# Optimization experiments

Hardware: AMD Instinct MI355X
Metric: run time of the kernel (lower is better)

Reference implementation:

```python
import jax, jax.numpy as jnp
import numpy as np

B, L, DIN, D = 16, 4096, 64, 64
HA, HL, WIN, NL, K, DFF = 8, 4, 64, 3, 3, 128


def _ln(x, g, b):
    m = x.mean(-1, keepdims=True)
    v = ((x - m) ** 2).mean(-1, keepdims=True)
    return (x - m) * jax.lax.rsqrt(v + 1e-5) * g + b


def _dynamic_conv(x, kernels, w1, b1, w2, b2):
    # x: (B, C, H, 1); kernels: (K, C_out, C_in, 3, 3)
    b, c, h, w = x.shape
    pooled = x.mean(axis=(2, 3))                      # AdaptiveAvgPool2d(1)
    hdn = jax.nn.relu(pooled @ w1.T + b1)             # 1x1 conv C -> C//4
    attn = jax.nn.softmax(hdn @ w2.T + b2, axis=-1)   # (B, K) kernel weights
    kw = kernels.reshape(K * c, c, 3, 3)              # run all K kernels in one conv
    out = jax.lax.conv_general_dilated(x, kw, (1, 1), [(1, 1), (1, 1)],
                                       dimension_numbers=('NCHW', 'OIHW', 'NCHW'))
    out = out.reshape(b, K, c, h, w)
    return jnp.einsum('bkchw,bk->bchw', out, attn)


def _agent_attn(x, wv, bv, an_bias, na_bias):
    # agent_num = 1: a single pooled agent token per sample
    b, n, c = x.shape
    hd = c // HA
    scale = hd ** -0.5
    v = x @ wv + bv
    lepe = v                                          # get_lepe uses the same linear
    qh = x.reshape(b, n, HA, hd).transpose(0, 2, 1, 3)  # (B, HA, L, hd)
    kh = qh
    vh = v.reshape(b, n, HA, hd).transpose(0, 2, 1, 3)
    agent = x.mean(axis=1).reshape(b, HA, 1, hd)      # AdaptiveAvgPool1d(1) over L
    a_attn = jax.nn.softmax(jnp.einsum('bhad,bhnd->bhan', agent * scale, kh) + an_bias, axis=-1)
    agent_v = jnp.einsum('bhan,bhnd->bhad', a_attn, vh)            # (B, HA, 1, hd)
    nb = jnp.swapaxes(na_bias, -1, -2)                              # (HA, L, 1)
    q_attn = jax.nn.softmax(jnp.einsum('bhnd,bhad->bhna', qh * scale, agent) + nb, axis=-1)
    out = jnp.einsum('bhna,bhad->bhnd', q_attn, agent_v)
    return out.transpose(0, 2, 1, 3).reshape(b, n, c) + lepe


def _local_attn(x, wq, bq, wk, bk, wv, bv, wo, bo):
    b, n, d = x.shape
    dk = d // HL
    nw = n // WIN

    def heads(w, bias):
        return (x @ w + bias).reshape(b, nw, WIN, HL, dk).transpose(0, 3, 1, 2, 4)

    q, k, v = heads(wq, bq), heads(wk, bk), heads(wv, bv)
    s = jnp.einsum('bhwid,bhwjd->bhwij', q, k) / (dk ** 0.5)        # per-window scores
    a = jax.nn.softmax(s, axis=-1)
    o = jnp.einsum('bhwij,bhwjd->bhwid', a, v)
    o = o.transpose(0, 2, 3, 1, 4).reshape(b, n, d)
    return o @ wo + bo


def setup_inputs() -> dict:
    key = jax.random.key(0)
    ks = iter(jax.random.split(key, 40))
    nrm = lambda shape, s=0.02: jax.random.normal(next(ks), shape, jnp.float32) * s
    Cr = DIN // 4
    return {
        'x': jax.random.normal(next(ks), (B, L, DIN), jnp.float32),
        'dc_kernels': nrm((3, K, DIN, DIN, 3, 3), 0.05),
        'dc_w1': nrm((3, Cr, DIN)), 'dc_b1': jnp.zeros((3, Cr), jnp.float32),
        'dc_w2': nrm((3, K, Cr)), 'dc_b2': jnp.zeros((3, K), jnp.float32),
        'emb_w': nrm((DIN, D)), 'emb_b': jnp.zeros((D,), jnp.float32),
        'getv_w': nrm((NL, D, D)), 'getv_b': jnp.zeros((NL, D), jnp.float32),
        'an_bias': nrm((NL, HA, 1, L)), 'na_bias': nrm((NL, HA, 1, L)),
        'wq': nrm((NL, D, D)), 'bq': jnp.zeros((NL, D), jnp.float32),
        'wk': nrm((NL, D, D)), 'bk': jnp.zeros((NL, D), jnp.float32),
        'wv': nrm((NL, D, D)), 'bv': jnp.zeros((NL, D), jnp.float32),
        'wo': nrm((NL, D, D)), 'bo': jnp.zeros((NL, D), jnp.float32),
        'ff_w1': nrm((NL, D, DFF)), 'ff_b1': jnp.zeros((NL, DFF), jnp.float32),
        'ff_w2': nrm((NL, DFF, D)), 'ff_b2': jnp.zeros((NL, D), jnp.float32),
        'ln1_g': jnp.ones((NL, D), jnp.float32), 'ln1_b': jnp.zeros((NL, D), jnp.float32),
        'ln2_g': jnp.ones((NL, D), jnp.float32), 'ln2_b': jnp.zeros((NL, D), jnp.float32),
    }


def reference(x, dc_kernels, dc_w1, dc_b1, dc_w2, dc_b2, emb_w, emb_b,
              getv_w, getv_b, an_bias, na_bias,
              wq, bq, wk, bk, wv, bv, wo, bo,
              ff_w1, ff_b1, ff_w2, ff_b2, ln1_g, ln1_b, ln2_g, ln2_b):
    # dynamic multi-kernel convs on (B, C=d_input, H=L, W=1)
    h = x.transpose(0, 2, 1)[..., None]
    for i in range(3):
        h = _dynamic_conv(h, dc_kernels[i], dc_w1[i], dc_b1[i], dc_w2[i], dc_b2[i])
    h = h[..., 0].transpose(0, 2, 1)
    # data embedding (value_linear=True, value_sqrt=False, pos_emb=False)
    h = h @ emb_w + emb_b
    for i in range(NL):
        attn = _agent_attn(h, getv_w[i], getv_b[i], an_bias[i], na_bias[i]) + \
               _local_attn(h, wq[i], bq[i], wk[i], bk[i], wv[i], bv[i], wo[i], bo[i])
        h1 = _ln(h + attn, ln1_g[i], ln1_b[i])
        ffo = jax.nn.relu(h1 @ ff_w1[i] + ff_b1[i]) @ ff_w2[i] + ff_b2[i]
        h = _ln(h1 + ffo, ln2_g[i], ln2_b[i])
    return h
```

## Files before the change

kernel.cpp:

```cpp
#include <hip/hip_runtime.h>

#define BB 16
#define LL 4096
#define DD 64

typedef const float* __restrict__ cfp;
typedef float* __restrict__ fp;
typedef const ushort* __restrict__ cup;
typedef ushort* __restrict__ up;

typedef __attribute__((ext_vector_type(8))) short bf16x8;
typedef __attribute__((ext_vector_type(4))) float f32x4;
#define MFMA16(a, b, c) __builtin_amdgcn_mfma_f32_16x16x32_bf16(a, b, c, 0, 0, 0)

__device__ __forceinline__ f32x4 zf4(){ f32x4 z; z[0]=0.f; z[1]=0.f; z[2]=0.f; z[3]=0.f; return z; }

union frag_u { bf16x8 v; uint2 u2[2]; uint u[4]; };

__device__ __forceinline__ float4 ld4(const float* p){ return *reinterpret_cast<const float4*>(p); }

__device__ __forceinline__ ushort f2bf(float f){
  uint u = __float_as_uint(f);
  return (ushort)((u + 0x7FFFu + ((u >> 16) & 1u)) >> 16);
}
__device__ __forceinline__ float bf2f(ushort u){
  return __uint_as_float(((uint)u) << 16);
}
__device__ __forceinline__ uint packf2(float a, float b){
  return (uint)f2bf(a) | ((uint)f2bf(b) << 16);
}
__device__ __forceinline__ uint2 pack4(float4 v){
  return make_uint2(packf2(v.x, v.y), packf2(v.z, v.w));
}
__device__ __forceinline__ bf16x8 ldfrag(const ushort* p){ return *reinterpret_cast<const bf16x8*>(p); }

__global__ __launch_bounds__(256) void k_pack(cfp wq, cfp wk, cfp wv, cfp getv, cfp wo,
                                              cfp fw1, cfp fw2, cfp embw,
                                              up dst, up dstE) {
  int layer = blockIdx.y;
  int e = blockIdx.x*256 + threadIdx.x;
  if (e >= 36864) {
    int rem = e - 36864;
    int j = rem & 7, lane = (rem >> 3) & 63, rest = rem >> 9;
    int nt = rest & 3, ks = rest >> 2;
    int k = ks*32 + ((lane >> 4) << 3) + j, n = nt*16 + (lane & 15);
    dstE[rem] = f2bf(embw[k*64 + n]);
    return;
  }
  const float* W; int N, rem;
  if (e < 20480) {
    int mm = e >> 12; rem = e & 4095;
    W = (mm==0?wq: mm==1?wk: mm==2?wv: mm==3?getv: wo) + layer*4096; N = 64;
  } else if (e < 28672) {
    rem = e - 20480; W = fw1 + layer*8192; N = 128;
  } else {
    rem = e - 28672; W = fw2 + layer*8192; N = 64;
  }
  int NT = N >> 4;
  int j = rem & 7, lane = (rem >> 3) & 63, rest = rem >> 9;
  int nt = rest % NT, ks = rest / NT;
  int k = ks*32 + ((lane >> 4) << 3) + j, n = nt*16 + (lane & 15);
  dst[(size_t)layer*36864 + e] = f2bf(W[(size_t)k*N + n]);
}

__global__ __launch_bounds__(256) void k_pool_part(cfp h, fp pp) {
  int b = blockIdx.x, gblk = blockIdx.y, t = threadIdx.x;
  int c = t & 63, r = t >> 6;
  const float* base = h + ((size_t)b*LL + (size_t)gblk*256)*64;
  float acc = 0.f;
  for (int l = r; l < 256; l += 4) acc += base[(size_t)l*64 + c];
  __shared__ float red[4][64];
  red[r][c] = acc; __syncthreads();
  if (t < 64) pp[(b*16 + gblk)*64 + t] = red[0][t]+red[1][t]+red[2][t]+red[3][t];
}

__device__ __forceinline__ void tiny_mlp3(int t, const float* __restrict__ pooled,
                                          cfp w1, cfp b1, cfp w2, cfp b2,
                                          float* attn, float* hdn) {
  if (t < 16) {
    float a = b1[t];
    for (int c = 0; c < 64; ++c) a += pooled[c]*w1[t*64 + c];
    hdn[t] = fmaxf(a, 0.f);
  }
  __syncthreads();
  if (t < 3) {
    float a = b2[t];
    for (int j = 0; j < 16; ++j) a += hdn[j]*w2[t*16 + j];
    attn[t] = a;
  }
  __syncthreads();
  if (t == 0) {
    float m = fmaxf(attn[0], fmaxf(attn[1], attn[2]));
    float e0 = __expf(attn[0]-m), e1 = __expf(attn[1]-m), e2 = __expf(attn[2]-m);
    float s = e0+e1+e2;
    attn[0]=e0/s; attn[1]=e1/s; attn[2]=e2/s;
  }
  __syncthreads();
}

__global__ __launch_bounds__(256) void k_attns(cfp pp, cfp x, cfp dcw1, cfp dcb1,
                                               cfp dcw2, cfp dcb2, cfp dck, fp attns) {
  int b = blockIdx.x, t = threadIdx.x;
  __shared__ float S[64], e0v[64], e1v[64], em0[64], em1[64];
  __shared__ float h10[64], h1m[64], Sn[64];
  __shared__ float pooled[64], hdn[16], attn[3], redu[256];
  const float* xb = x + (size_t)b*LL*64;
  if (t < 64) {
    float s = 0.f;
    for (int g = 0; g < 16; ++g) s += pp[((size_t)b*16 + g)*64 + t];
    S[t] = s;
    pooled[t] = s * (1.f/4096.f);
    e0v[t] = xb[t];
    e1v[t] = xb[64 + t];
    em0[t] = xb[(size_t)(LL-2)*64 + t];
    em1[t] = xb[(size_t)(LL-1)*64 + t];
  }
  __syncthreads();
  tiny_mlp3(t, pooled, dcw1, dcb1, dcw2, dcb2, attn, hdn);
  if (t < 3) attns[b*9 + t] = attn[t];
  {
    int co = t & 63, q = t >> 6;
    float a0 = attn[0], a1 = attn[1], a2 = attn[2];
    float ph0=0.f, phm=0.f, pS=0.f;
    cfp kb = dck;
    for (int ci = q*16; ci < q*16 + 16; ++ci) {
      size_t base = ((size_t)co*64 + ci)*9 + 1;
      float k00=kb[base],       k01=kb[base+3],       k02=kb[base+6];
      float k10=kb[base+36864], k11=kb[base+36867],   k12=kb[base+36870];
      float k20=kb[base+73728], k21=kb[base+73731],   k22=kb[base+73734];
      float w0 = a0*k00 + a1*k10 + a2*k20;
      float w1 = a0*k01 + a1*k11 + a2*k21;
      float w2 = a0*k02 + a1*k12 + a2*k22;
      ph0 += w1*e0v[ci] + w2*e1v[ci];
      phm += w0*em0[ci] + w1*em1[ci];
      pS  += w0*(S[ci]-em1[ci]) + w1*S[ci] + w2*(S[ci]-e0v[ci]);
    }
    redu[t] = ph0; __syncthreads();
    if (t < 64) h10[t] = redu[t]+redu[64+t]+redu[128+t]+redu[192+t];
    __syncthreads();
    redu[t] = phm; __syncthreads();
    if (t < 64) h1m[t] = redu[t]+redu[64+t]+redu[128+t]+redu[192+t];
    __syncthreads();
    redu[t] = pS; __syncthreads();
    if (t < 64) {
      Sn[t] = redu[t]+redu[64+t]+redu[128+t]+redu[192+t];
      pooled[t] = Sn[t] * (1.f/4096.f);
    }
    __syncthreads();
  }
  tiny_mlp3(t, pooled, dcw1+1024, dcb1+16, dcw2+48, dcb2+3, attn, hdn);
  if (t < 3) attns[b*9 + 3 + t] = attn[t];
  {
    int co = t & 63, q = t >> 6;
    float a0 = attn[0], a1 = attn[1], a2 = attn[2];
    float pS = 0.f;
    cfp kb = dck + 110592;
    for (int ci = q*16; ci < q*16 + 16; ++ci) {
      size_t base = ((size_t)co*64 + ci)*9 + 1;
      float k00=kb[base],       k01=kb[base+3],       k02=kb[base+6];
      float k10=kb[base+36864], k11=kb[base+36867],   k12=kb[base+36870];
      float k20=kb[base+73728], k21=kb[base+73731],   k22=kb[base+73734];
      float w0 = a0*k00 + a1*k10 + a2*k20;
      float w1 = a0*k01 + a1*k11 + a2*k21;
      float w2 = a0*k02 + a1*k12 + a2*k22;
      pS += w0*(Sn[ci]-h1m[ci]) + w1*Sn[ci] + w2*(Sn[ci]-h10[ci]);
    }
    redu[t] = pS; __syncthreads();
    if (t < 64) pooled[t] = (redu[t]+redu[64+t]+redu[128+t]+redu[192+t]) * (1.f/4096.f);
    __syncthreads();
  }
  tiny_mlp3(t, pooled, dcw1+2048, dcb1+32, dcw2+96, dcb2+6, attn, hdn);
  if (t < 3) attns[b*9 + 6 + t] = attn[t];
}

__global__ __launch_bounds__(256) void k_wefff(cfp attns, cfp dck, up weffB) {
  int b = blockIdx.x, stage = blockIdx.y >> 3, slice = blockIdx.y & 7, t = threadIdx.x;
  float a0 = attns[b*9 + stage*3 + 0];
  float a1 = attns[b*9 + stage*3 + 1];
  float a2 = attns[b*9 + stage*3 + 2];
  cfp kern = dck + (size_t)stage*110592;
  int e0i = slice*1536;
  for (int e = e0i + t; e < e0i + 1536; e += 256) {
    int j = e & 7, lane = (e >> 3) & 63, nt = (e >> 9) & 3, ks = e >> 11;
    int k = ks*32 + ((lane >> 4) << 3) + j;
    int co = nt*16 + (lane & 15);
    int kh = k >> 6, ci = k & 63;
    size_t base = ((size_t)co*64 + ci)*9 + kh*3 + 1;
    float v = a0*kern[base] + a1*kern[base + 36864] + a2*kern[base + 2*36864];
    weffB[((size_t)stage*16 + b)*12288 + e] = f2bf(v);
  }
}

__device__ __forceinline__ void conv_mfma(const ushort* Ts, const ushort* wb,
                                          int band, int lr, int lg, int l, f32x4 acc[4]) {
  #pragma unroll
  for (int nt = 0; nt < 4; ++nt) acc[nt] = zf4();
  #pragma unroll
  for (int ks = 0; ks < 6; ++ks) {
    int k8 = ks*32 + lg*8;
    int kh = k8 >> 6, ci = k8 & 63;
    bf16x8 a = ldfrag(Ts + (band + lr + kh)*72 + ci);
    #pragma unroll
    for (int nt = 0; nt < 4; ++nt)
      acc[nt] = MFMA16(a, ldfrag(wb + ((ks*4+nt)*64 + l)*8), acc[nt]);
  }
}

__global__ __launch_bounds__(256) void k_convF(cfp x, cup weffB, cup wE, cfp embb,
                                               up houtB, fp pp) {
  int b = blockIdx.x, wblk = blockIdx.y, t = threadIdx.x;
  int n0 = wblk*64;
  __shared__ ushort TsA[84*72];
  __shared__ ushort TsB[84*72];
  __shared__ float red[64*17];
  int w = t >> 6, l = t & 63, lr = l & 15, lg = l >> 4;

  for (int idx = t; idx < 1344; idx += 256) {
    int r = idx >> 4, c4 = (idx & 15)*4;
    int g = n0 - 4 + r;
    float4 v = make_float4(0.f,0.f,0.f,0.f);
    if (r >= 1 && r <= 70 && g >= 0 && g < LL) v = ld4(x + ((size_t)b*LL + g)*64 + c4);
    *(uint2*)(TsA + r*72 + c4) = pack4(v);
  }
  for (int idx = t; idx < 32; idx += 256) {
    int r = 82 + (idx >> 4), c4 = (idx & 15)*4;
    *(uint2*)(TsB + r*72 + c4) = make_uint2(0u,0u);
  }
  __syncthreads();

  {
    const ushort* wb = weffB + (size_t)b*12288;
    for (int bi = w; bi < 5; bi += 4) {
      int band = 2 + bi*16;
      f32x4 acc[4];
      conv_mfma(TsA, wb, band - 1, lr, lg, l, acc);
      #pragma unroll
      for (int nt = 0; nt < 4; ++nt)
        #pragma unroll
        for (int reg = 0; reg < 4; ++reg) {
          int row = band + lg*4 + reg;
          int g = n0 - 4 + row;
          float v = (g >= 0 && g < LL) ? acc[nt][reg] : 0.f;
          TsB[row*72 + nt*16 + lr] = f2bf(v);
        }
    }
  }
  __syncthreads();
  {
    const ushort* wb = weffB + (size_t)(16 + b)*12288;
    for (int bi = w; bi < 5; bi += 4) {
      int band = 3 + bi*16;
      f32x4 acc[4];
      conv_mfma(TsB, wb, band - 1, lr, lg, l, acc);
      #pragma unroll
      for (int nt = 0; nt < 4; ++nt)
        #pragma unroll
        for (int reg = 0; reg < 4; ++reg) {
          int row = band + lg*4 + reg;
          int g = n0 - 4 + row;
          float v = (g >= 0 && g < LL) ? acc[nt][reg] : 0.f;
          TsA[row*72 + nt*16 + lr] = f2bf(v);
        }
    }
  }
  __syncthreads();
  {
    const ushort* wb = weffB + (size_t)(32 + b)*12288;
    int band = 4 + w*16;
    f32x4 acc[4];
    conv_mfma(TsA, wb, band - 1, lr, lg, l, acc);
    #pragma unroll
    for (int nt = 0; nt < 4; ++nt)
      #pragma unroll
      for (int reg = 0; reg < 4; ++reg)
        TsB[(band + lg*4 + reg)*72 + nt*16 + lr] = f2bf(acc[nt][reg]);
  }
  __syncthreads();
  {
    int band = 4 + w*16;
    f32x4 ea[4];
    #pragma unroll
    for (int nt = 0; nt < 4; ++nt) ea[nt] = zf4();
    #pragma unroll
    for (int ks = 0; ks < 2; ++ks) {
      bf16x8 a = ldfrag(TsB + (band + lr)*72 + ks*32 + lg*8);
      #pragma unroll
      for (int nt = 0; nt < 4; ++nt)
        ea[nt] = MFMA16(a, ldfrag(wE + ((ks*4+nt)*64 + l)*8), ea[nt]);
    }
    #pragma unroll
    for (int nt = 0; nt < 4; ++nt) {
      int col = nt*16 + lr;
      float bc = embb[col], part = 0.f;
      #pragma unroll
      for (int reg = 0; reg < 4; ++reg) {
        int row = band + lg*4 + reg;
        float y = ea[nt][reg] + bc;
        TsA[row*72 + col] = f2bf(y);
        part += y;
      }
      red[col*17 + w*4 + lg] = part;
    }
  }
  __syncthreads();
  for (int idx = t; idx < 512; idx += 256) {
    int r = idx >> 3, c8 = (idx & 7)*8;
    *(uint4*)(houtB + ((size_t)b*LL + n0 + r)*64 + c8) = *(const uint4*)(TsA + (r+4)*72 + c8);
  }
  if (t < 64) {
    float s = 0.f;
    #pragma unroll
    for (int g = 0; g < 16; ++g) s += red[t*17 + g];
    pp[((size_t)b*64 + wblk)*64 + t] = s;
  }
}

__global__ __launch_bounds__(256) void k_agent2(cup h16, cfp anb, cfp pp,
                                                fp pm, fp pe, fp pw) {
  int b = blockIdx.x, ch = blockIdx.y, t = threadIdx.x;
  int w = t >> 6, l = t & 63;
  __shared__ float means_s[64];
  __shared__ float sc[8][258];
  __shared__ float red4[4][64];
  __shared__ float esp[8][33];
  __shared__ float mcs[8], ess[8];
  __shared__ float wred[4][8][64];
  {
    float acc = 0.f;
    for (int c = w; c < 64; c += 4) acc += pp[((size_t)b*64 + c)*64 + l];
    red4[w][l] = acc;
  }
  __syncthreads();
  if (t < 64) means_s[t] = (red4[0][t]+red4[1][t]+red4[2][t]+red4[3][t])
                           * (1.f/4096.f) * 0.35355339059327373f;
  __syncthreads();
  const ushort* hb = h16 + ((size_t)b*LL + (size_t)ch*256)*64;
  int g8 = l >> 3, k8 = l & 7;
  float ms8[8];
  #pragma unroll
  for (int j = 0; j < 8; ++j) ms8[j] = means_s[k8*8 + j];
  #pragma unroll
  for (int it = 0; it < 8; ++it) {
    int n = w*64 + it*8 + g8;
    uint4 hv = *(const uint4*)(hb + (size_t)n*64 + k8*8);
    float d = bf2f((ushort)(hv.x & 0xffffu))*ms8[0] + bf2f((ushort)(hv.x >> 16))*ms8[1]
            + bf2f((ushort)(hv.y & 0xffffu))*ms8[2] + bf2f((ushort)(hv.y >> 16))*ms8[3]
            + bf2f((ushort)(hv.z & 0xffffu))*ms8[4] + bf2f((ushort)(hv.z >> 16))*ms8[5]
            + bf2f((ushort)(hv.w & 0xffffu))*ms8[6] + bf2f((ushort)(hv.w >> 16))*ms8[7];
    sc[k8][n] = d;
  }
  __syncthreads();
  int hh = t >> 5, j0 = (t & 31) * 8;
  const float* ab = anb + (size_t)hh*LL + ch*256 + j0;
  float loc[8];
  float mx = -1e30f;
  #pragma unroll
  for (int k = 0; k < 8; ++k) {
    loc[k] = sc[hh][j0 + k] + ab[k];
    mx = fmaxf(mx, loc[k]);
  }
  esp[hh][t & 31] = mx;
  __syncthreads();
  if (t < 8) {
    float m = -1e30f;
    for (int k = 0; k < 32; ++k) m = fmaxf(m, esp[t][k]);
    mcs[t] = m;
  }
  __syncthreads();
  {
    float M = mcs[hh], s = 0.f;
    #pragma unroll
    for (int k = 0; k < 8; ++k) {
      float e = __expf(loc[k] - M);
      sc[hh][j0 + k] = e;
      s += e;
    }
    esp[hh][t & 31] = s;
  }
  __syncthreads();
  if (t < 8) {
    float s = 0.f;
    for (int k = 0; k < 32; ++k) s += esp[t][k];
    ess[t] = s;
  }
  float acc8[8] = {};
  for (int i = 0; i < 64; ++i) {
    int n = w*64 + i;
    float xv = bf2f(hb[(size_t)n*64 + l]);
    #pragma unroll
    for (int q = 0; q < 8; ++q) acc8[q] = fmaf(sc[q][n], xv, acc8[q]);
  }
  __syncthreads();
  #pragma unroll
  for (int q = 0; q < 8; ++q) wred[w][q][l] = acc8[q];
  __syncthreads();
  for (int o = t; o < 512; o += 256) {
    int q = o >> 6, ll = o & 63;
    pw[(((size_t)b*16 + ch)*8 + q)*64 + ll] =
        wred[0][q][ll]+wred[1][q][ll]+wred[2][q][ll]+wred[3][q][ll];
  }
  if (t < 8) {
    pe[((size_t)b*16 + ch)*8 + t] = ess[t];
    pm[((size_t)b*16 + ch)*8 + t] = mcs[t];
  }
}

template<bool OUT_BF16>
__global__ __launch_bounds__(256, 4) void k_layer(
    cup h16, cfp pm, cfp pe, cfp pw, cfp getv, cfp getvb, cup wB,
    cfp bq, cfp bk, cfp bv, cfp bo,
    cfp g1, cfp be1, cfp b1, cfp b2, cfp g2, cfp be2,
    fp Y, up Y16, fp pp) {
  __shared__ float smem[10048];
  ushort* HsB  = (ushort*)(smem);
  ushort* Qp   = (ushort*)(smem + 2304);
  ushort* Kp   = (ushort*)(smem + 4864);
  ushort* Vt   = (ushort*)(smem + 7424);
  float*  sums = smem + 9728;
  float*  agvs = smem + 9984;
  float*  wm   = smem + 7424;
  float*  msden= smem + 7944;
  ushort* OB   = (ushort*)(smem + 7424);
  float*  red  = smem + 7424;
  ushort* HidB = (ushort*)(smem + 2304);

  int t = threadIdx.x;
  size_t n0 = (size_t)blockIdx.x*64;
  int b = (int)(n0 >> 12);
  int w = t >> 6, l = t & 63, band = w*16, lr = l & 15, lg = l >> 4;

  #pragma unroll
  for (int it = 0; it < 2; ++it) {
    int idx = it*256 + t, r = idx >> 3, c8 = (idx & 7)*8;
    *(uint4*)(HsB + r*72 + c8) = *(const uint4*)(h16 + (n0 + r)*64 + c8);
  }
  if (t < 8) {
    float M = -1e30f;
    for (int c = 0; c < 16; ++c) M = fmaxf(M, pm[((size_t)b*16+c)*8 + t]);
    float d = 0.f;
    for (int c = 0; c < 16; ++c)
      d += pe[((size_t)b*16+c)*8 + t] * __expf(pm[((size_t)b*16+c)*8 + t] - M);
    msden[t] = M; msden[8+t] = d;
  }
  __syncthreads();
  for (int o = t; o < 512; o += 256) {
    int q = o >> 6, l2 = o & 63;
    float M = msden[q], s = 0.f;
    for (int c = 0; c < 16; ++c)
      s += pw[(((size_t)b*16+c)*8 + q)*64 + l2] * __expf(pm[((size_t)b*16+c)*8 + q] - M);
    wm[q*65 + l2] = s / msden[8+q];
  }
  __syncthreads();
  if (t < 64) {
    int q = t >> 3;
    float a = getvb[t];
    for (int c = 0; c < 64; ++c) a = fmaf(wm[q*65 + c], getv[c*64 + t], a);
    agvs[t] = a;
  }
  __syncthreads();

  f32x4 ka[4], va[4], qa[4], la[4];
  #pragma unroll
  for (int nt = 0; nt < 4; ++nt) {
    ka[nt] = zf4(); va[nt] = zf4(); qa[nt] = zf4(); la[nt] = zf4();
  }
  #pragma unroll
  for (int ks = 0; ks < 2; ++ks) {
    bf16x8 a = ldfrag(HsB + (band + lr)*72 + ks*32 + lg*8);
    #pragma unroll
    for (int nt = 0; nt < 4; ++nt) {
      int fo = ((ks*4 + nt)*64 + l)*8;
      qa[nt] = MFMA16(a, ldfrag(wB + fo),         qa[nt]);
      ka[nt] = MFMA16(a, ldfrag(wB + 4096 + fo),  ka[nt]);
      va[nt] = MFMA16(a, ldfrag(wB + 8192 + fo),  va[nt]);
      la[nt] = MFMA16(a, ldfrag(wB + 12288 + fo), la[nt]);
    }
  }
  #pragma unroll
  for (int nt = 0; nt < 4; ++nt) {
    int col = nt*16 + lr;
    float bkc = bk[col], bvc = bv[col], bqc = bq[col];
    #pragma unroll
    for (int reg = 0; reg < 4; ++reg) {
      int tok = band + 4*lg + reg;
      Kp[nt*1280 + tok*20 + lr] = f2bf(ka[nt][reg] + bkc);
      Qp[nt*1280 + tok*20 + lr] = f2bf((qa[nt][reg] + bqc) * 0.25f);
    }
    int tok0 = band + 4*lg;
    *(uint2*)(Vt + nt*1152 + lr*72 + tok0) =
        make_uint2(packf2(va[nt][0]+bvc, va[nt][1]+bvc),
                   packf2(va[nt][2]+bvc, va[nt][3]+bvc));
  }
  __syncthreads();

  {
    frag_u kaf[4], qbf[4], vbf[4], pf;
    #pragma unroll
    for (int tt = 0; tt < 4; ++tt) {
      kaf[tt].u2[0] = *(const uint2*)(Kp + w*1280 + (tt*16+lr)*20 + lg*4);
      kaf[tt].u[2] = 0; kaf[tt].u[3] = 0;
      qbf[tt].u2[0] = *(const uint2*)(Qp + w*1280 + (tt*16+lr)*20 + lg*4);
      qbf[tt].u[2] = 0; qbf[tt].u[3] = 0;
      vbf[tt].u2[0] = *(const uint2*)(Vt + w*1152 + lr*72 + tt*16 + lg*4);
      vbf[tt].u[2] = 0; vbf[tt].u[3] = 0;
    }
    f32x4 st[4][4];
    #pragma unroll
    for (int kt = 0; kt < 4; ++kt)
      #pragma unroll
      for (int qt = 0; qt < 4; ++qt) {
        f32x4 z = zf4();
        st[kt][qt] = MFMA16(kaf[kt].v, qbf[qt].v, z);
      }
    f32x4 oacc[4];
    #pragma unroll
    for (int qt = 0; qt < 4; ++qt) {
      float M = -1e30f;
      #pragma unroll
      for (int kt = 0; kt < 4; ++kt)
        #pragma unroll
        for (int reg = 0; reg < 4; ++reg) M = fmaxf(M, st[kt][qt][reg]);
      M = fmaxf(M, __shfl_xor(M, 16));
      M = fmaxf(M, __shfl_xor(M, 32));
      float s = 0.f;
      #pragma unroll
      for (int kt = 0; kt < 4; ++kt)
        #pragma unroll
        for (int reg = 0; reg < 4; ++reg) {
          float e = __expf(st[kt][qt][reg] - M);
          st[kt][qt][reg] = e; s += e;
        }
      s += __shfl_xor(s, 16);
      s += __shfl_xor(s, 32);
      if (lg == 0) sums[w*64 + qt*16 + lr] = s;
      oacc[qt] = zf4();
    }
    #pragma unroll
    for (int qt = 0; qt < 4; ++qt)
      #pragma unroll
      for (int kt = 0; kt < 4; ++kt) {
        pf.u[0] = packf2(st[kt][qt][0], st[kt][qt][1]);
        pf.u[1] = packf2(st[kt][qt][2], st[kt][qt][3]);
        pf.u[2] = 0; pf.u[3] = 0;
        oacc[qt] = MFMA16(pf.v, vbf[kt].v, oacc[qt]);
      }
    __syncthreads();
    #pragma unroll
    for (int qt = 0; qt < 4; ++qt)
      #pragma unroll
      for (int reg = 0; reg < 4; ++reg) {
        int q = qt*16 + 4*lg + reg;
        OB[q*72 + band + lr] = f2bf(oacc[qt][reg] / sums[w*64 + q]);
      }
  }
  __syncthreads();

  float comb[4][4];
  {
    f32x4 wa[4];
    #pragma unroll
    for (int nt = 0; nt < 4; ++nt) wa[nt] = zf4();
    #pragma unroll
    for (int ks = 0; ks < 2; ++ks) {
      bf16x8 a = ldfrag(OB + (band + lr)*72 + ks*32 + lg*8);
      #pragma unroll
      for (int nt = 0; nt < 4; ++nt)
        wa[nt] = MFMA16(a, ldfrag(wB + 16384 + ((ks*4+nt)*64 + l)*8), wa[nt]);
    }
    #pragma unroll
    for (int nt = 0; nt < 4; ++nt) {
      int col = nt*16 + lr;
      float cadd = bo[col] + agvs[col] + getvb[col];
      #pragma unroll
      for (int reg = 0; reg < 4; ++reg) {
        int row = band + lg*4 + reg;
        comb[nt][reg] = wa[nt][reg] + la[nt][reg] + cadd + bf2f(HsB[row*72 + col]);
      }
    }
  }
  {
    float mean1[4], rstd1[4];
    #pragma unroll
    for (int reg = 0; reg < 4; ++reg) {
      float s = comb[0][reg]+comb[1][reg]+comb[2][reg]+comb[3][reg];
      float qq = comb[0][reg]*comb[0][reg]+comb[1][reg]*comb[1][reg]
               + comb[2][reg]*comb[2][reg]+comb[3][reg]*comb[3][reg];
      s += __shfl_xor(s,1); qq += __shfl_xor(qq,1);
      s += __shfl_xor(s,2); qq += __shfl_xor(qq,2);
      s += __shfl_xor(s,4); qq += __shfl_xor(qq,4);
      s += __shfl_xor(s,8); qq += __shfl_xor(qq,8);
      float mn = s*0.015625f;
      mean1[reg] = mn;
      rstd1[reg] = rsqrtf(qq*0.015625f - mn*mn + 1e-5f);
    }
    #pragma unroll
    for (int nt = 0; nt < 4; ++nt) {
      int col = nt*16 + lr;
      float gg = g1[col], bb = be1[col];
      #pragma unroll
      for (int reg = 0; reg < 4; ++reg) {
        int row = band + lg*4 + reg;
        float h1 = (comb[nt][reg]-mean1[reg])*rstd1[reg]*gg + bb;
        HsB[row*72 + col] = f2bf(h1);
      }
    }
  }
  __syncthreads();

  {
    f32x4 fa[8];
    #pragma unroll
    for (int nt = 0; nt < 8; ++nt) fa[nt] = zf4();
    #pragma unroll
    for (int ks = 0; ks < 2; ++ks) {
      bf16x8 a = ldfrag(HsB + (band + lr)*72 + ks*32 + lg*8);
      #pragma unroll
      for (int nt = 0; nt < 8; ++nt)
        fa[nt] = MFMA16(a, ldfrag(wB + 20480 + ((ks*8+nt)*64 + l)*8), fa[nt]);
    }
    #pragma unroll
    for (int nt = 0; nt < 8; ++nt) {
      int col = nt*16 + lr;
      float b1c = b1[col];
      #pragma unroll
      for (int reg = 0; reg < 4; ++reg) {
        int row = band + lg*4 + reg;
        HidB[row*136 + col] = f2bf(fmaxf(fa[nt][reg] + b1c, 0.f));
      }
    }
  }
  __syncthreads();

  {
    f32x4 f2[4];
    #pragma unroll
    for (int nt = 0; nt < 4; ++nt) f2[nt] = zf4();
    #pragma unroll
    for (int ks = 0; ks < 4; ++ks) {
      bf16x8 a = ldfrag(HidB + (band + lr)*136 + ks*32 + lg*8);
      #pragma unroll
      for (int nt = 0; nt < 4; ++nt)
        f2[nt] = MFMA16(a, ldfrag(wB + 28672 + ((ks*4+nt)*64 + l)*8), f2[nt]);
    }
    float c2[4][4];
    #pragma unroll
    for (int nt = 0; nt < 4; ++nt) {
      int col = nt*16 + lr;
      float b2c = b2[col];
      #pragma unroll
      for (int reg = 0; reg < 4; ++reg) {
        int row = band + lg*4 + reg;
        c2[nt][reg] = f2[nt][reg] + b2c + bf2f(HsB[row*72 + col]);
      }
    }
    float mean2[4], rstd2[4];
    #pragma unroll
    for (int reg = 0; reg < 4; ++reg) {
      float s = c2[0][reg]+c2[1][reg]+c2[2][reg]+c2[3][reg];
      float qq = c2[0][reg]*c2[0][reg]+c2[1][reg]*c2[1][reg]
               + c2[2][reg]*c2[2][reg]+c2[3][reg]*c2[3][reg];
      s += __shfl_xor(s,1); qq += __shfl_xor(qq,1);
      s += __shfl_xor(s,2); qq += __shfl_xor(qq,2);
      s += __shfl_xor(s,4); qq += __shfl_xor(qq,4);
      s += __shfl_xor(s,8); qq += __shfl_xor(qq,8);
      float mn = s*0.015625f;
      mean2[reg] = mn;
      rstd2[reg] = rsqrtf(qq*0.015625f - mn*mn + 1e-5f);
    }
    __syncthreads();
    #pragma unroll
    for (int nt = 0; nt < 4; ++nt) {
      int col = nt*16 + lr;
      float gg = g2[col], bb = be2[col];
      float part = 0.f;
      #pragma unroll
      for (int reg = 0; reg < 4; ++reg) {
        int row = band + lg*4 + reg;
        float y = (c2[nt][reg]-mean2[reg])*rstd2[reg]*gg + bb;
        if (OUT_BF16) Y16[(n0 + row)*64 + col] = f2bf(y);
        else          Y[(n0 + row)*64 + col] = y;
        part += y;
      }
      red[col*17 + w*4 + lg] = part;
    }
  }
  __syncthreads();
  if (t < 64) {
    float s = 0.f;
    #pragma unroll
    for (int g = 0; g < 16; ++g) s += red[t*17 + g];
    pp[(size_t)blockIdx.x*64 + t] = s;
  }
}

extern "C" void kernel_launch(void* const* d_in, const int* in_sizes, int n_in,
                              void* d_out, int out_size, void* d_ws, size_t ws_size,
                              hipStream_t stream) {
  (void)in_sizes; (void)n_in; (void)out_size; (void)ws_size;
  const float* x    = (const float*)d_in[0];
  const float* dck  = (const float*)d_in[1];
  const float* dcw1 = (const float*)d_in[2];
  const float* dcb1 = (const float*)d_in[3];
  const float* dcw2 = (const float*)d_in[4];
  const float* dcb2 = (const float*)d_in[5];
  const float* embw = (const float*)d_in[6];
  const float* embb = (const float*)d_in[7];
  const float* getvw= (const float*)d_in[8];
  const float* getvb= (const float*)d_in[9];
  const float* anb  = (const float*)d_in[10];
  const float* wq = (const float*)d_in[12]; const float* bq = (const float*)d_in[13];
  const float* wk = (const float*)d_in[14]; const float* bk = (const float*)d_in[15];
  const float* wv = (const float*)d_in[16]; const float* bv = (const float*)d_in[17];
  const float* wo = (const float*)d_in[18]; const float* bo = (const float*)d_in[19];
  const float* fw1= (const float*)d_in[20]; const float* fb1= (const float*)d_in[21];
  const float* fw2= (const float*)d_in[22]; const float* fb2= (const float*)d_in[23];
  const float* g1 = (const float*)d_in[24]; const float* be1= (const float*)d_in[25];
  const float* g2 = (const float*)d_in[26]; const float* be2= (const float*)d_in[27];

  float* out = (float*)d_out;
  float* ws  = (float*)d_ws;
  float* pp    = ws;
  float* pm    = pp + 65536;
  float* pe    = pm + 2048;
  float* pw    = pe + 2048;
  float* attns = pw + 131072;
  ushort* hB0  = (ushort*)(attns + 256);
  ushort* hB1  = hB0 + (size_t)BB*LL*64;
  ushort* weffB= hB1 + (size_t)BB*LL*64;
  ushort* wsB  = weffB + (size_t)3*BB*12288;
  ushort* wsE  = wsB + (size_t)3*36864;

  dim3 blk(256);
  const int NT = BB*LL/64;

  k_pack<<<dim3(160, 3), blk, 0, stream>>>(wq, wk, wv, getvw, wo, fw1, fw2, embw, wsB, wsE);
  k_pool_part<<<dim3(BB,16), blk, 0, stream>>>(x, pp);
  k_attns<<<BB, blk, 0, stream>>>(pp, x, dcw1, dcb1, dcw2, dcb2, dck, attns);
  k_wefff<<<dim3(BB,24), blk, 0, stream>>>(attns, dck, weffB);
  k_convF<<<dim3(BB,64), blk, 0, stream>>>(x, weffB, wsE, embb, hB0, pp);

  ushort* h  = hB0;
  ushort* hn = hB1;
  for (int i = 0; i < 3; ++i) {
    k_agent2<<<dim3(BB,16), blk, 0, stream>>>(h, anb + (size_t)i*8*4096, pp, pm, pe, pw);
    if (i == 2) {
      k_layer<false><<<NT, blk, 0, stream>>>(h, pm, pe, pw, getvw + i*4096, getvb + i*64,
                                             wsB + (size_t)i*36864,
                                             bq + i*64, bk + i*64, bv + i*64, bo + i*64,
                                             g1 + i*64, be1 + i*64, fb1 + i*128, fb2 + i*64,
                                             g2 + i*64, be2 + i*64, out, nullptr, pp);
    } else {
      k_layer<true><<<NT, blk, 0, stream>>>(h, pm, pe, pw, getvw + i*4096, getvb + i*64,
                                            wsB + (size_t)i*36864,
                                            bq + i*64, bk + i*64, bv + i*64, bo + i*64,
                                            g1 + i*64, be1 + i*64, fb1 + i*128, fb2 + i*64,
                                            g2 + i*64, be2 + i*64, nullptr, hn, pp);
    }
    ushort* tmp = h; h = hn; hn = tmp;
  }
}
```

Before: 211.1 us.

## Precompute per-kernel conv pooled sums to parallelize dynamic-conv attention chain

The serial single-block-per-sample attention computation is split into kernels that precompute, for each candidate conv kernel, the pooled sums and boundary terms independently of the softmax weights. Linearity then lets the final attention kernel combine them with cheap weighted sums. This removes the long serial weight loads from the critical path and spreads them over more blocks, at the cost of two extra kernel launches and more total arithmetic (nine combinations for stage two).

```diff
diff --git a/kernel.cpp b/kernel.cpp
--- a/kernel.cpp
+++ b/kernel.cpp
@@ -98,77 +98,96 @@
   __syncthreads();
 }
 
-__global__ __launch_bounds__(256) void k_attns(cfp pp, cfp x, cfp dcw1, cfp dcb1,
-                                               cfp dcw2, cfp dcb2, cfp dck, fp attns) {
-  int b = blockIdx.x, t = threadIdx.x;
+__global__ __launch_bounds__(256) void k_prep0(cfp pp, cfp x, cfp dck, fp R0) {
+  int b = blockIdx.x, k = blockIdx.y, t = threadIdx.x;
   __shared__ float S[64], e0v[64], e1v[64], em0[64], em1[64];
-  __shared__ float h10[64], h1m[64], Sn[64];
-  __shared__ float pooled[64], hdn[16], attn[3], redu[256];
+  __shared__ float redu[3][256];
   const float* xb = x + (size_t)b*LL*64;
   if (t < 64) {
     float s = 0.f;
     for (int g = 0; g < 16; ++g) s += pp[((size_t)b*16 + g)*64 + t];
     S[t] = s;
+    e0v[t] = xb[t]; e1v[t] = xb[64 + t];
+    em0[t] = xb[(size_t)(LL-2)*64 + t]; em1[t] = xb[(size_t)(LL-1)*64 + t];
+  }
+  __syncthreads();
+  int co = t & 63, q = t >> 6;
+  cfp kb = dck + (size_t)k*36864;
+  float pS = 0.f, ph0 = 0.f, phm = 0.f;
+  for (int ci = q*16; ci < q*16 + 16; ++ci) {
+    size_t base = ((size_t)co*64 + ci)*9 + 1;
+    float w0 = kb[base], w1 = kb[base+3], w2 = kb[base+6];
+    pS  += w0*(S[ci]-em1[ci]) + w1*S[ci] + w2*(S[ci]-e0v[ci]);
+    ph0 += w1*e0v[ci] + w2*e1v[ci];
+    phm += w0*em0[ci] + w1*em1[ci];
+  }
+  redu[0][t] = pS; redu[1][t] = ph0; redu[2][t] = phm;
+  __syncthreads();
+  if (t < 64) {
+    R0[((b*3 + 0)*3 + k)*64 + t] = redu[0][t]+redu[0][64+t]+redu[0][128+t]+redu[0][192+t];
+    R0[((b*3 + 1)*3 + k)*64 + t] = redu[1][t]+redu[1][64+t]+redu[1][128+t]+redu[1][192+t];
+    R0[((b*3 + 2)*3 + k)*64 + t] = redu[2][t]+redu[2][64+t]+redu[2][128+t]+redu[2][192+t];
+  }
+}
+
+__global__ __launch_bounds__(256) void k_prep1(cfp R0, cfp dck, fp T1) {
+  int b = blockIdx.x, k = blockIdx.y / 3, k0 = blockIdx.y % 3, t = threadIdx.x;
+  __shared__ float u0[64], u1[64], u2[64];
+  __shared__ float redu[256];
+  if (t < 64) {
+    float rs  = R0[((b*3 + 0)*3 + k0)*64 + t];
+    float rh0 = R0[((b*3 + 1)*3 + k0)*64 + t];
+    float rhm = R0[((b*3 + 2)*3 + k0)*64 + t];
+    u0[t] = rs - rhm; u1[t] = rs; u2[t] = rs - rh0;
+  }
+  __syncthreads();
+  int co = t & 63, q = t >> 6;
+  cfp kb = dck + 110592 + (size_t)k*36864;
+  float pS = 0.f;
+  for (int ci = q*16; ci < q*16 + 16; ++ci) {
+    size_t base = ((size_t)co*64 + ci)*9 + 1;
+    pS += kb[base]*u0[ci] + kb[base+3]*u1[ci] + kb[base+6]*u2[ci];
+  }
+  redu[t] = pS;
+  __syncthreads();
+  if (t < 64)
+    T1[((size_t)b*9 + blockIdx.y)*64 + t] = redu[t]+redu[64+t]+redu[128+t]+redu[192+t];
+}
+
+__global__ __launch_bounds__(256) void k_attns2(cfp pp, cfp R0, cfp T1,
+                                                cfp dcw1, cfp dcb1, cfp dcw2, cfp dcb2,
+                                                fp attns) {
+  int b = blockIdx.x, t = threadIdx.x;
+  __shared__ float pooled[64], hdn[16], attn[3], a0s[3], a1s[3];
+  if (t < 64) {
+    float s = 0.f;
+    for (int g = 0; g < 16; ++g) s += pp[((size_t)b*16 + g)*64 + t];
     pooled[t] = s * (1.f/4096.f);
-    e0v[t] = xb[t];
-    e1v[t] = xb[64 + t];
-    em0[t] = xb[(size_t)(LL-2)*64 + t];
-    em1[t] = xb[(size_t)(LL-1)*64 + t];
   }
   __syncthreads();
   tiny_mlp3(t, pooled, dcw1, dcb1, dcw2, dcb2, attn, hdn);
-  if (t < 3) attns[b*9 + t] = attn[t];
-  {
-    int co = t & 63, q = t >> 6;
-    float a0 = attn[0], a1 = attn[1], a2 = attn[2];
-    float ph0=0.f, phm=0.f, pS=0.f;
-    cfp kb = dck;
-    for (int ci = q*16; ci < q*16 + 16; ++ci) {
-      size_t base = ((size_t)co*64 + ci)*9 + 1;
-      float k00=kb[base],       k01=kb[base+3],       k02=kb[base+6];
-      float k10=kb[base+36864], k11=kb[base+36867],   k12=kb[base+36870];
-      float k20=kb[base+73728], k21=kb[base+73731],   k22=kb[base+73734];
-      float w0 = a0*k00 + a1*k10 + a2*k20;
-      float w1 = a0*k01 + a1*k11 + a2*k21;
-      float w2 = a0*k02 + a1*k12 + a2*k22;
-      ph0 += w1*e0v[ci] + w2*e1v[ci];
-      phm += w0*em0[ci] + w1*em1[ci];
-      pS  += w0*(S[ci]-em1[ci]) + w1*S[ci] + w2*(S[ci]-e0v[ci]);
-    }
-    redu[t] = ph0; __syncthreads();
-    if (t < 64) h10[t] = redu[t]+redu[64+t]+redu[128+t]+redu[192+t];
-    __syncthreads();
-    redu[t] = phm; __syncthreads();
-    if (t < 64) h1m[t] = redu[t]+redu[64+t]+redu[128+t]+redu[192+t];
-    __syncthreads();
-    redu[t] = pS; __syncthreads();
-    if (t < 64) {
-      Sn[t] = redu[t]+redu[64+t]+redu[128+t]+redu[192+t];
-      pooled[t] = Sn[t] * (1.f/4096.f);
-    }
-    __syncthreads();
-  }
+  if (t < 3) { attns[b*9 + t] = attn[t]; a0s[t] = attn[t]; }
+  __syncthreads();
+  if (t < 64) {
+    float sn = a0s[0]*R0[((b*3+0)*3 + 0)*64 + t]
+             + a0s[1]*R0[((b*3+0)*3 + 1)*64 + t]
+             + a0s[2]*R0[((b*3+0)*3 + 2)*64 + t];
+    pooled[t] = sn * (1.f/4096.f);
+  }
+  __syncthreads();
   tiny_mlp3(t, pooled, dcw1+1024, dcb1+16, dcw2+48, dcb2+3, attn, hdn);
-  if (t < 3) attns[b*9 + 3 + t] = attn[t];
-  {
-    int co = t & 63, q = t >> 6;
-    float a0 = attn[0], a1 = attn[1], a2 = attn[2];
-    float pS = 0.f;
-    cfp kb = dck + 110592;
-    for (int ci = q*16; ci < q*16 + 16; ++ci) {
-      size_t base = ((size_t)co*64 + ci)*9 + 1;
-      float k00=kb[base],       k01=kb[base+3],       k02=kb[base+6];
-      float k10=kb[base+36864], k11=kb[base+36867],   k12=kb[base+36870];
-      float k20=kb[base+73728], k21=kb[base+73731],   k22=kb[base+73734];
-      float w0 = a0*k00 + a1*k10 + a2*k20;
-      float w1 = a0*k01 + a1*k11 + a2*k21;
-      float w2 = a0*k02 + a1*k12 + a2*k22;
-      pS += w0*(Sn[ci]-h1m[ci]) + w1*Sn[ci] + w2*(Sn[ci]-h10[ci]);
-    }
-    redu[t] = pS; __syncthreads();
-    if (t < 64) pooled[t] = (redu[t]+redu[64+t]+redu[128+t]+redu[192+t]) * (1.f/4096.f);
-    __syncthreads();
-  }
+  if (t < 3) { attns[b*9 + 3 + t] = attn[t]; a1s[t] = attn[t]; }
+  __syncthreads();
+  if (t < 64) {
+    float s2 = 0.f;
+    #pragma unroll
+    for (int k = 0; k < 3; ++k)
+      #pragma unroll
+      for (int k0 = 0; k0 < 3; ++k0)
+        s2 += a1s[k]*a0s[k0]*T1[((size_t)b*9 + k*3 + k0)*64 + t];
+    pooled[t] = s2 * (1.f/4096.f);
+  }
+  __syncthreads();
   tiny_mlp3(t, pooled, dcw1+2048, dcb1+32, dcw2+96, dcb2+6, attn, hdn);
   if (t < 3) attns[b*9 + 6 + t] = attn[t];
 }
@@ -724,7 +743,9 @@
   float* pe    = pm + 2048;
   float* pw    = pe + 2048;
   float* attns = pw + 131072;
-  ushort* hB0  = (ushort*)(attns + 256);
+  float* R0    = attns + 256;
+  float* T1    = R0 + 9216;
+  ushort* hB0  = (ushort*)(T1 + 9216);
   ushort* hB1  = hB0 + (size_t)BB*LL*64;
   ushort* weffB= hB1 + (size_t)BB*LL*64;
   ushort* wsB  = weffB + (size_t)3*BB*12288;
@@ -735,7 +756,9 @@
 
   k_pack<<<dim3(160, 3), blk, 0, stream>>>(wq, wk, wv, getvw, wo, fw1, fw2, embw, wsB, wsE);
   k_pool_part<<<dim3(BB,16), blk, 0, stream>>>(x, pp);
-  k_attns<<<BB, blk, 0, stream>>>(pp, x, dcw1, dcb1, dcw2, dcb2, dck, attns);
+  k_prep0<<<dim3(BB,3), blk, 0, stream>>>(pp, x, dck, R0);
+  k_prep1<<<dim3(BB,9), blk, 0, stream>>>(R0, dck, T1);
+  k_attns2<<<BB, blk, 0, stream>>>(pp, R0, T1, dcw1, dcb1, dcw2, dcb2, attns);
   k_wefff<<<dim3(BB,24), blk, 0, stream>>>(attns, dck, weffB);
   k_convF<<<dim3(BB,64), blk, 0, stream>>>(x, weffB, wsE, embb, hB0, pp);
 
```

Result: faster. 190.6 us (-9.7%).
